# Performance work log

Hardware: AMD Instinct MI355X
Metric: run time of the kernel (lower is better)

Reference implementation:

```python
import jax, jax.numpy as jnp
import numpy as np

NEG = -1e30  # log-space 'zero'


def _lse3(a, b, c):
    m = jnp.maximum(jnp.maximum(a, b), c)
    return m + jnp.log(jnp.exp(a - m) + jnp.exp(b - m) + jnp.exp(c - m))


def _ctc_loss_sum(logp, targets, input_lens, target_lens, blank=0):
    # logp: (T, B, C) log-probabilities; targets: (B, S) int; lens: (B,) int
    T, B, C = logp.shape
    S = targets.shape[1]
    L = 2 * S + 1
    # Extended label sequence: blank, t0, blank, t1, ..., blank  -> (B, L)
    ext = jnp.full((B, L), blank, dtype=targets.dtype).at[:, 1::2].set(targets)
    # Skip transition (l-2 -> l) allowed only for non-blank labels differing from l-2
    allow_skip = jnp.concatenate(
        [jnp.zeros((B, 2), bool), (ext[:, 2:] != blank) & (ext[:, 2:] != ext[:, :-2])],
        axis=1)  # (B, L)
    pos = jnp.arange(L)[None, :]
    valid = pos < (2 * target_lens[:, None] + 1)  # (B, L) mask of used trellis columns

    def emit(lp_t):  # (B, C) -> (B, L): log-prob of emitting ext label at each position
        return jnp.take_along_axis(lp_t, ext, axis=1)

    e0 = emit(logp[0])
    alpha0 = jnp.full((B, L), NEG, logp.dtype).at[:, 0].set(e0[:, 0]).at[:, 1].set(e0[:, 1])
    alpha0 = jnp.where(valid, alpha0, NEG)

    def step(alpha, lp_t):
        a1 = jnp.pad(alpha[:, :-1], ((0, 0), (1, 0)), constant_values=NEG)
        a2 = jnp.pad(alpha[:, :-2], ((0, 0), (2, 0)), constant_values=NEG)
        a2 = jnp.where(allow_skip, a2, NEG)
        new = _lse3(alpha, a1, a2) + emit(lp_t)
        new = jnp.where(valid, new, NEG)
        return new, new

    _, alphas = jax.lax.scan(step, alpha0, logp[1:])
    alphas = jnp.concatenate([alpha0[None], alphas], axis=0)  # (T, B, L)

    # Per-sequence final alpha at t = input_len - 1
    a_fin = alphas[input_lens - 1, jnp.arange(B)]  # (B, L)
    end_blank = jnp.take_along_axis(a_fin, (2 * target_lens)[:, None], axis=1)[:, 0]
    end_label = jnp.take_along_axis(a_fin, (2 * target_lens - 1)[:, None], axis=1)[:, 0]
    m = jnp.maximum(end_blank, end_label)
    loss = -(m + jnp.log(jnp.exp(end_blank - m) + jnp.exp(end_label - m)))  # (B,)
    # zero_infinity=True: replace (near-)infinite losses with 0
    loss = jnp.where(loss > -0.5 * NEG, 0.0, loss)
    # reduction='none' followed by .sum() in the module
    return loss.sum()


def setup_inputs() -> dict:
    key = jax.random.key(0)
    T, B, C, S = 1000, 32, 1000, 100
    k1, k2 = jax.random.split(key)
    logits = jax.random.normal(k1, (T, B, C), dtype=jnp.float32)
    logp = jax.nn.log_softmax(logits, axis=-1)  # CTCLoss expects log-softmax input
    targets = jax.random.randint(k2, (B, S), 1, C)  # labels in [1, C), never blank(0)
    input_lens = jnp.full((B,), T, dtype=jnp.int32)
    target_lens = jnp.full((B,), S, dtype=jnp.int32)
    return {"logp": logp, "targets": targets, "input_lens": input_lens, "target_lens": target_lens}


def reference(logp, targets, input_lens, target_lens):
    return _ctc_loss_sum(logp, targets, input_lens, target_lens, blank=0)
```

## Files before the change

### kernel.cpp

```cpp
#include <hip/hip_runtime.h>
#include <hip/hip_fp16.h>


constexpr int T = 1000, B = 32, C = 1000, S = 100;
constexpr int L = 2 * S + 1;
constexpr int RS = 204;
constexpr int PFD = 32;
constexpr int RROWS = T + PFD;
constexpr float OFF = 7.0f;
constexpr float LOG2E = 1.4426950408889634f;
constexpr float LN2 = 0.6931471805599453f;

__device__ __forceinline__ float dpp_shr1(float x) {
    return __int_as_float(
        __builtin_amdgcn_update_dpp(0, __float_as_int(x), 0x138, 0xF, 0xF, true));
}

__device__ __forceinline__ float wave_max_nonneg(float x) {
#define DPP_MAX(ctrl)                                                        \
    x = fmaxf(x, __int_as_float(__builtin_amdgcn_update_dpp(                 \
                     0, __float_as_int(x), (ctrl), 0xF, 0xF, true)))
    DPP_MAX(0x111);
    DPP_MAX(0x112);
    DPP_MAX(0x114);
    DPP_MAX(0x118);
    DPP_MAX(0x142);
    DPP_MAX(0x143);
#undef DPP_MAX
    return __int_as_float(__builtin_amdgcn_readlane(__float_as_int(x), 63));
}

__global__ void __launch_bounds__(256) stage_kernel(
        const float* __restrict__ logp, const int* __restrict__ targets,
        float* __restrict__ ws) {
    const int t = blockIdx.x * 4 + (threadIdx.x >> 6);
    const int b = blockIdx.y;
    const int lane = threadIdx.x & 63;
    if (lane > 50) return;
    const int col = 4 * lane;
    const float* row = logp + ((size_t)t * B + b) * C;

    const float pb = exp2f((row[0] + OFF) * LOG2E);
    float p1 = 0.f, p3 = 0.f;
    const int l1 = col + 1;
    if (l1 < L) p1 = exp2f((row[targets[b * S + (l1 >> 1)]] + OFF) * LOG2E);
    const int l3 = col + 3;
    if (l3 < L) p3 = exp2f((row[targets[b * S + (l3 >> 1)]] + OFF) * LOG2E);

    float4 v;
    v.x = pb;
    v.y = p1;
    v.z = (col + 2 < L) ? pb : 0.f;
    v.w = p3;
    *reinterpret_cast<float4*>(ws + ((size_t)b * RROWS + t) * RS + col) = v;
}

__global__ void __launch_bounds__(64, 1) ctc_kernel(
        const float* __restrict__ ws, const int* __restrict__ targets,
        const int* __restrict__ input_lens, const int* __restrict__ target_lens,
        float* __restrict__ out) {
    const int b = blockIdx.x;
    const int lane = threadIdx.x;
    const int col = (lane <= 50) ? 4 * lane : 200;
    const int Tb = input_lens[b];
    const int tl = target_lens[b];
    const float* pw = ws + (size_t)b * RROWS * RS;

    float m1 = 0.f, m3 = 0.f;
    if (lane <= 50) {
        const int l1 = col + 1;
        if (l1 >= 3 && l1 < L) {
            const int s = (l1 - 1) >> 1;
            if (targets[b * S + s] != targets[b * S + s - 1]) m1 = 1.f;
        }
        const int l3 = col + 3;
        if (l3 >= 3 && l3 < L) {
            const int s = (l3 - 1) >> 1;
            if (targets[b * S + s] != targets[b * S + s - 1]) m3 = 1.f;
        }
    }

    float a0 = 0.f, a1 = 0.f, a2 = 0.f, a3 = 0.f;
    {
        const float4 q0 = *reinterpret_cast<const float4*>(pw + col);
        if (lane == 0) { a0 = q0.x; a1 = q0.y; }
    }
    int esum = 0;

#define CTC_STEP(Q_)                                  \
    do {                                              \
        const float am1 = dpp_shr1(a3);               \
        const float s01 = a0 + a1;                    \
        const float s23 = a2 + a3;                    \
        const float n0 = (a0 + am1) * (Q_).x;         \
        const float n1 = fmaf(am1, m1, s01) * (Q_).y; \
        const float n2 = (a1 + a2) * (Q_).z;          \
        const float n3 = fmaf(a1, m3, s23) * (Q_).w;  \
        a0 = n0; a1 = n1; a2 = n2; a3 = n3;           \
    } while (0)

#define CTC_RESCALE()                                                          \
    do {                                                                       \
        const float mx = wave_max_nonneg(fmaxf(fmaxf(a0, a1), fmaxf(a2, a3))); \
        const unsigned bits = __float_as_uint(mx);                             \
        if (bits != 0u) {                                                      \
            const int e = (int)((bits >> 23) & 0xFFu) - 127;                   \
            const float sc = __uint_as_float((unsigned)(127 - e) << 23);       \
            a0 *= sc; a1 *= sc; a2 *= sc; a3 *= sc;                            \
            esum += e;                                                         \
        }                                                                      \
    } while (0)

    float4 P[PFD];
    {
        const float* pf0 = pw + (size_t)RS + col;
#pragma unroll
        for (int i = 0; i < PFD; ++i)
            P[i] = *reinterpret_cast<const float4*>(pf0 + (size_t)i * RS);
    }
    const float* pf = pw + (size_t)(PFD + 1) * RS + col;

    int t = 1;
    while (t + PFD <= Tb) {
#pragma unroll
        for (int i = 0; i < PFD; ++i) {
            const float4 q = P[i];
            P[i] = *reinterpret_cast<const float4*>(pf);
            pf += RS;
            CTC_STEP(q);
            if (i == 15) CTC_RESCALE();
        }
        CTC_RESCALE();
        t += PFD;
    }
    {
        const int rem = Tb - t;
#pragma unroll
        for (int i = 0; i < PFD; ++i) {
            if (i < rem) {
                const float4 q = P[i];
                CTC_STEP(q);
                if (i == 15) CTC_RESCALE();
            }
        }
    }
#undef CTC_STEP

    const int e1 = 2 * tl, e2 = 2 * tl - 1;
    float contrib = 0.f;
    if (lane <= 50) {
        if (col + 0 == e1 || col + 0 == e2) contrib += a0;
        if (col + 1 == e1 || col + 1 == e2) contrib += a1;
        if (col + 2 == e1 || col + 2 == e2) contrib += a2;
        if (col + 3 == e1 || col + 3 == e2) contrib += a3;
    }
#pragma unroll
    for (int off = 32; off; off >>= 1) contrib += __shfl_xor(contrib, off);

    if (lane == 0) {
        const float logalpha = logf(contrib) + (float)esum * LN2 - OFF * (float)Tb;
        float loss = -logalpha;
        if (!(loss < 0.5e30f)) loss = 0.f;
        atomicAdd(out, loss);
    }
}

__global__ void __launch_bounds__(64, 1) ctc_direct_kernel(
        const float* __restrict__ logp, const int* __restrict__ targets,
        const int* __restrict__ input_lens, const int* __restrict__ target_lens,
        float* __restrict__ out) {
    const int b = blockIdx.x;
    const int lane = threadIdx.x;
    const int col = (lane <= 50) ? 4 * lane : 200;
    const int Tb = input_lens[b];
    const int tl = target_lens[b];

    int cc[4]; float mm[4], pm[4];
#pragma unroll
    for (int i = 0; i < 4; ++i) {
        const int l = col + i;
        const bool real = (lane <= 50) && (l < L);
        pm[i] = real ? 1.f : 0.f;
        cc[i] = real ? ((l & 1) ? targets[b * S + (l >> 1)] : 0) : 0;
        float mk = 0.f;
        if (real && (l & 1) && l >= 3) {
            const int s = (l - 1) >> 1;
            if (targets[b * S + s] != targets[b * S + s - 1]) mk = 1.f;
        }
        mm[i] = mk;
    }
    const float m1 = mm[1], m3 = mm[3];

    float a0 = 0.f, a1 = 0.f, a2 = 0.f, a3 = 0.f;
    {
        const float* rowp = logp + (size_t)b * C;
        const float p0 = pm[0] * exp2f((rowp[cc[0]] + OFF) * LOG2E);
        const float p1 = pm[1] * exp2f((rowp[cc[1]] + OFF) * LOG2E);
        if (lane == 0) { a0 = p0; a1 = p1; }
    }
    int esum = 0;

    for (int t = 1; t < Tb; ++t) {
        const float* rowp = logp + ((size_t)t * B + b) * C;
        const float p0 = pm[0] * exp2f((rowp[cc[0]] + OFF) * LOG2E);
        const float p1 = pm[1] * exp2f((rowp[cc[1]] + OFF) * LOG2E);
        const float p2 = pm[2] * exp2f((rowp[cc[2]] + OFF) * LOG2E);
        const float p3 = pm[3] * exp2f((rowp[cc[3]] + OFF) * LOG2E);
        const float am1 = dpp_shr1(a3);
        const float n0 = (a0 + am1) * p0;
        const float n1 = fmaf(am1, m1, a0 + a1) * p1;
        const float n2 = (a1 + a2) * p2;
        const float n3 = fmaf(a1, m3, a2 + a3) * p3;
        a0 = n0; a1 = n1; a2 = n2; a3 = n3;
        if ((t & 15) == 0) {
            const float mx = wave_max_nonneg(fmaxf(fmaxf(a0, a1), fmaxf(a2, a3)));
            const unsigned bits = __float_as_uint(mx);
            if (bits != 0u) {
                const int e = (int)((bits >> 23) & 0xFFu) - 127;
                const float sc = __uint_as_float((unsigned)(127 - e) << 23);
                a0 *= sc; a1 *= sc; a2 *= sc; a3 *= sc;
                esum += e;
            }
        }
    }

    const int e1 = 2 * tl, e2 = 2 * tl - 1;
    float contrib = 0.f;
    if (lane <= 50) {
        if (col + 0 == e1 || col + 0 == e2) contrib += a0;
        if (col + 1 == e1 || col + 1 == e2) contrib += a1;
        if (col + 2 == e1 || col + 2 == e2) contrib += a2;
        if (col + 3 == e1 || col + 3 == e2) contrib += a3;
    }
#pragma unroll
    for (int off = 32; off; off >>= 1) contrib += __shfl_xor(contrib, off);
    if (lane == 0) {
        const float logalpha = logf(contrib) + (float)esum * LN2 - OFF * (float)Tb;
        float loss = -logalpha;
        if (!(loss < 0.5e30f)) loss = 0.f;
        atomicAdd(out, loss);
    }
}

extern "C" void kernel_launch(void* const* d_in, const int* in_sizes, int n_in,
                              void* d_out, int out_size, void* d_ws, size_t ws_size,
                              hipStream_t stream) {
    (void)in_sizes; (void)n_in; (void)out_size;
    const float* logp = (const float*)d_in[0];
    const int* targets = (const int*)d_in[1];
    const int* input_lens = (const int*)d_in[2];
    const int* target_lens = (const int*)d_in[3];
    float* out = (float*)d_out;
    float* ws = (float*)d_ws;

    hipMemsetAsync(d_out, 0, sizeof(float), stream);

    const size_t ws_needed = (size_t)B * RROWS * RS * sizeof(float);
    if (ws_size >= ws_needed) {
        dim3 gA(T / 4, B);
        stage_kernel<<<gA, 256, 0, stream>>>(logp, targets, ws);
        ctc_kernel<<<B, 64, 0, stream>>>(ws, targets, input_lens, target_lens, out);
    } else {
        ctc_direct_kernel<<<B, 64, 0, stream>>>(logp, targets, input_lens,
                                                target_lens, out);
    }
}
```

Measured before the change: 234.9 us.

## Merge staging and CTC recursion into one cooperative kernel with grid sync

Replaces the memset plus the two launches (staging kernel, recursion kernel) with a single cooperative kernel. Each of its 1024 waves stages a contiguous time segment for one batch item, then a grid sync hands off to 32 waves that run the recursion, and a second grid sync precedes a deterministic serial sum of the losses. This removes launch gaps and the atomic/memset, but grid syncs have their own cost and staging now uses only 256 blocks. The old multi-kernel path remains as a fallback if the cooperative launch fails.

New measurement: 308.1 us. 1.31x slower.

```diff
diff --git a/kernel.cpp b/kernel.cpp
--- a/kernel.cpp
+++ b/kernel.cpp
@@ -1,6 +1,8 @@
 #include <hip/hip_runtime.h>
-#include <hip/hip_fp16.h>
-
+#include <hip/hip_cooperative_groups.h>
+
+
+namespace cg = cooperative_groups;
 
 constexpr int T = 1000, B = 32, C = 1000, S = 100;
 constexpr int L = 2 * S + 1;
@@ -10,6 +12,15 @@
 constexpr float OFF = 7.0f;
 constexpr float LOG2E = 1.4426950408889634f;
 constexpr float LN2 = 0.6931471805599453f;
+
+constexpr int GBLK = 256;
+constexpr int WPB = 4;
+constexpr int NW = GBLK * WPB;
+constexpr int WAVES_PER_B = NW / B;
+constexpr int TSEG = (T + WAVES_PER_B - 1) / WAVES_PER_B;
+static_assert(NW % B == 0, "wave mapping");
+
+constexpr size_t DATA_WORDS = (size_t)B * RROWS * RS;
 
 __device__ __forceinline__ float dpp_shr1(float x) {
     return __int_as_float(
@@ -30,41 +41,10 @@
     return __int_as_float(__builtin_amdgcn_readlane(__float_as_int(x), 63));
 }
 
-__global__ void __launch_bounds__(256) stage_kernel(
-        const float* __restrict__ logp, const int* __restrict__ targets,
-        float* __restrict__ ws) {
-    const int t = blockIdx.x * 4 + (threadIdx.x >> 6);
-    const int b = blockIdx.y;
-    const int lane = threadIdx.x & 63;
-    if (lane > 50) return;
-    const int col = 4 * lane;
-    const float* row = logp + ((size_t)t * B + b) * C;
-
-    const float pb = exp2f((row[0] + OFF) * LOG2E);
-    float p1 = 0.f, p3 = 0.f;
-    const int l1 = col + 1;
-    if (l1 < L) p1 = exp2f((row[targets[b * S + (l1 >> 1)]] + OFF) * LOG2E);
-    const int l3 = col + 3;
-    if (l3 < L) p3 = exp2f((row[targets[b * S + (l3 >> 1)]] + OFF) * LOG2E);
-
-    float4 v;
-    v.x = pb;
-    v.y = p1;
-    v.z = (col + 2 < L) ? pb : 0.f;
-    v.w = p3;
-    *reinterpret_cast<float4*>(ws + ((size_t)b * RROWS + t) * RS + col) = v;
-}
-
-__global__ void __launch_bounds__(64, 1) ctc_kernel(
-        const float* __restrict__ ws, const int* __restrict__ targets,
-        const int* __restrict__ input_lens, const int* __restrict__ target_lens,
-        float* __restrict__ out) {
-    const int b = blockIdx.x;
-    const int lane = threadIdx.x;
+__device__ float ctc_wave_loss(const float* __restrict__ pw,
+                               const int* __restrict__ targets, int b, int Tb,
+                               int tl, int lane) {
     const int col = (lane <= 50) ? 4 * lane : 200;
-    const int Tb = input_lens[b];
-    const int tl = target_lens[b];
-    const float* pw = ws + (size_t)b * RROWS * RS;
 
     float m1 = 0.f, m3 = 0.f;
     if (lane <= 50) {
@@ -145,6 +125,7 @@
         }
     }
 #undef CTC_STEP
+#undef CTC_RESCALE
 
     const int e1 = 2 * tl, e2 = 2 * tl - 1;
     float contrib = 0.f;
@@ -157,12 +138,119 @@
 #pragma unroll
     for (int off = 32; off; off >>= 1) contrib += __shfl_xor(contrib, off);
 
-    if (lane == 0) {
-        const float logalpha = logf(contrib) + (float)esum * LN2 - OFF * (float)Tb;
-        float loss = -logalpha;
-        if (!(loss < 0.5e30f)) loss = 0.f;
-        atomicAdd(out, loss);
-    }
+    const float logalpha = logf(contrib) + (float)esum * LN2 - OFF * (float)Tb;
+    float loss = -logalpha;
+    if (!(loss < 0.5e30f)) loss = 0.f;
+    return loss;
+}
+
+__global__ void __launch_bounds__(256, 1) ctc_coop_kernel(
+        const float* __restrict__ logp, const int* __restrict__ targets,
+        const int* __restrict__ input_lens, const int* __restrict__ target_lens,
+        float* __restrict__ ws, float* __restrict__ out) {
+    const int lane = threadIdx.x & 63;
+    const int wv = threadIdx.x >> 6;
+    float* loss_slot = ws + DATA_WORDS;
+
+    {
+        const int gw = blockIdx.x * WPB + wv;
+        const int b = gw / WAVES_PER_B;
+        const int seg = gw % WAVES_PER_B;
+        const int t0 = seg * TSEG;
+        const int t1 = min(t0 + TSEG, T);
+        const int col = 4 * lane;
+        const bool ln = (lane <= 50);
+        const bool h1 = ln && (col + 1 < L);
+        const bool h3 = ln && (col + 3 < L);
+        const int c1 = h1 ? targets[b * S + 2 * lane] : 0;
+        const int c3 = h3 ? targets[b * S + 2 * lane + 1] : 0;
+        float* wb = ws + (size_t)b * RROWS * RS;
+
+        for (int t = t0; t < t1; t += 4) {
+            const int n = min(4, t1 - t);
+            float f0[4], fa[4], fb[4];
+#pragma unroll
+            for (int j = 0; j < 4; ++j) {
+                if (j < n) {
+                    const float* row = logp + ((size_t)(t + j) * B + b) * C;
+                    f0[j] = row[0];
+                    fa[j] = h1 ? row[c1] : 0.f;
+                    fb[j] = h3 ? row[c3] : 0.f;
+                }
+            }
+#pragma unroll
+            for (int j = 0; j < 4; ++j) {
+                if (j < n && ln) {
+                    const float pb = exp2f((f0[j] + OFF) * LOG2E);
+                    const float p1 = h1 ? exp2f((fa[j] + OFF) * LOG2E) : 0.f;
+                    const float p3 = h3 ? exp2f((fb[j] + OFF) * LOG2E) : 0.f;
+                    float4 v;
+                    v.x = pb;
+                    v.y = p1;
+                    v.z = (col + 2 < L) ? pb : 0.f;
+                    v.w = p3;
+                    *reinterpret_cast<float4*>(wb + (size_t)(t + j) * RS + col) = v;
+                }
+            }
+        }
+    }
+
+    cg::this_grid().sync();
+
+    if (blockIdx.x < (unsigned)B && wv == 0) {
+        const int b = blockIdx.x;
+        const int Tb = min(input_lens[b], T);
+        const int tl = target_lens[b];
+        const float* pw = ws + (size_t)b * RROWS * RS;
+        const float loss = ctc_wave_loss(pw, targets, b, Tb, tl, lane);
+        if (lane == 0) loss_slot[b] = loss;
+    }
+
+    cg::this_grid().sync();
+
+    if (blockIdx.x == 0 && threadIdx.x == 0) {
+        float s = 0.f;
+        for (int i = 0; i < B; ++i) s += loss_slot[i];
+        out[0] = s;
+    }
+}
+
+__global__ void __launch_bounds__(256) stage_kernel(
+        const float* __restrict__ logp, const int* __restrict__ targets,
+        float* __restrict__ ws) {
+    const int t = blockIdx.x * 4 + (threadIdx.x >> 6);
+    const int b = blockIdx.y;
+    const int lane = threadIdx.x & 63;
+    if (lane > 50) return;
+    const int col = 4 * lane;
+    const float* row = logp + ((size_t)t * B + b) * C;
+
+    const float pb = exp2f((row[0] + OFF) * LOG2E);
+    float p1 = 0.f, p3 = 0.f;
+    const int l1 = col + 1;
+    if (l1 < L) p1 = exp2f((row[targets[b * S + (l1 >> 1)]] + OFF) * LOG2E);
+    const int l3 = col + 3;
+    if (l3 < L) p3 = exp2f((row[targets[b * S + (l3 >> 1)]] + OFF) * LOG2E);
+
+    float4 v;
+    v.x = pb;
+    v.y = p1;
+    v.z = (col + 2 < L) ? pb : 0.f;
+    v.w = p3;
+    *reinterpret_cast<float4*>(ws + ((size_t)b * RROWS + t) * RS + col) = v;
+}
+
+__global__ void __launch_bounds__(64, 1) ctc_kernel(
+        const float* __restrict__ ws, const int* __restrict__ targets,
+        const int* __restrict__ input_lens, const int* __restrict__ target_lens,
+        float* __restrict__ out) {
+    const int b = blockIdx.x;
+    const int lane = threadIdx.x;
+    const int Tb = input_lens[b];
+    const int tl = target_lens[b];
+    const float* pw = ws + (size_t)b * RROWS * RS;
+    const float loss = ctc_wave_loss(pw, targets, b, Tb, tl, lane);
+    if (lane == 0) atomicAdd(out, loss);
 }
 
 __global__ void __launch_bounds__(64, 1) ctc_direct_kernel(
@@ -253,14 +341,19 @@
     float* out = (float*)d_out;
     float* ws = (float*)d_ws;
 
-    hipMemsetAsync(d_out, 0, sizeof(float), stream);
-
-    const size_t ws_needed = (size_t)B * RROWS * RS * sizeof(float);
+    const size_t ws_needed = (DATA_WORDS + (size_t)B) * sizeof(float);
     if (ws_size >= ws_needed) {
+        void* args[] = {(void*)&logp, (void*)&targets, (void*)&input_lens,
+                        (void*)&target_lens, (void*)&ws, (void*)&out};
+        const hipError_t err = hipLaunchCooperativeKernel(
+            (const void*)ctc_coop_kernel, dim3(GBLK), dim3(256), args, 0, stream);
+        if (err == hipSuccess) return;
+        hipMemsetAsync(d_out, 0, sizeof(float), stream);
         dim3 gA(T / 4, B);
         stage_kernel<<<gA, 256, 0, stream>>>(logp, targets, ws);
         ctc_kernel<<<B, 64, 0, stream>>>(ws, targets, input_lens, target_lens, out);
     } else {
+        hipMemsetAsync(d_out, 0, sizeof(float), stream);
         ctc_direct_kernel<<<B, 64, 0, stream>>>(logp, targets, input_lens,
                                                 target_lens, out);
     }
```

## Stage logp rows through LDS with coalesced loads and fold output zeroing

Applied to the files above, without the earlier changes.

The staging kernel now assigns one block per (t,b) row. It copies the full 1000-float row into shared memory with coalesced float4 loads and computes each trellis column's scaled probability from LDS, writing one float per thread. This replaces the previous scattered global gathers of target entries. The output memset is folded into the staging kernel, which saves an API call/launch, and Tb is clamped to T. The trade-off is that the whole row is read (about 4KB versus roughly 400B of gathers), and the grid uses four times as many blocks, each with many idle threads.

Measured after the change: 228.7 us. 2.6% less time.

```diff
diff --git a/kernel.cpp b/kernel.cpp
--- a/kernel.cpp
+++ b/kernel.cpp
@@ -1,5 +1,4 @@
 #include <hip/hip_runtime.h>
-#include <hip/hip_fp16.h>
 
 
 constexpr int T = 1000, B = 32, C = 1000, S = 100;
@@ -10,6 +9,8 @@
 constexpr float OFF = 7.0f;
 constexpr float LOG2E = 1.4426950408889634f;
 constexpr float LN2 = 0.6931471805599453f;
+
+constexpr size_t DATA_WORDS = (size_t)B * RROWS * RS;
 
 __device__ __forceinline__ float dpp_shr1(float x) {
     return __int_as_float(
@@ -32,27 +33,27 @@
 
 __global__ void __launch_bounds__(256) stage_kernel(
         const float* __restrict__ logp, const int* __restrict__ targets,
-        float* __restrict__ ws) {
-    const int t = blockIdx.x * 4 + (threadIdx.x >> 6);
+        float* __restrict__ ws, float* __restrict__ out) {
+    const int t = blockIdx.x;
     const int b = blockIdx.y;
-    const int lane = threadIdx.x & 63;
-    if (lane > 50) return;
-    const int col = 4 * lane;
-    const float* row = logp + ((size_t)t * B + b) * C;
-
-    const float pb = exp2f((row[0] + OFF) * LOG2E);
-    float p1 = 0.f, p3 = 0.f;
-    const int l1 = col + 1;
-    if (l1 < L) p1 = exp2f((row[targets[b * S + (l1 >> 1)]] + OFF) * LOG2E);
-    const int l3 = col + 3;
-    if (l3 < L) p3 = exp2f((row[targets[b * S + (l3 >> 1)]] + OFF) * LOG2E);
-
-    float4 v;
-    v.x = pb;
-    v.y = p1;
-    v.z = (col + 2 < L) ? pb : 0.f;
-    v.w = p3;
-    *reinterpret_cast<float4*>(ws + ((size_t)b * RROWS + t) * RS + col) = v;
+    __shared__ float row[C];
+    const float* src = logp + ((size_t)t * B + b) * C;
+    const int tid = threadIdx.x;
+    if (tid < C / 4) {
+        ((float4*)row)[tid] = ((const float4*)src)[tid];
+    }
+    __syncthreads();
+    if (t == 0 && b == 0 && tid == 0) out[0] = 0.f;
+    if (tid < RS) {
+        float p;
+        if (tid < L) {
+            const int c = (tid & 1) ? targets[b * S + (tid >> 1)] : 0;
+            p = exp2f((row[c] + OFF) * LOG2E);
+        } else {
+            p = 0.0f;
+        }
+        ws[((size_t)b * RROWS + t) * RS + tid] = p;
+    }
 }
 
 __global__ void __launch_bounds__(64, 1) ctc_kernel(
@@ -62,7 +63,7 @@
     const int b = blockIdx.x;
     const int lane = threadIdx.x;
     const int col = (lane <= 50) ? 4 * lane : 200;
-    const int Tb = input_lens[b];
+    const int Tb = min(input_lens[b], T);
     const int tl = target_lens[b];
     const float* pw = ws + (size_t)b * RROWS * RS;
 
@@ -145,6 +146,7 @@
         }
     }
 #undef CTC_STEP
+#undef CTC_RESCALE
 
     const int e1 = 2 * tl, e2 = 2 * tl - 1;
     float contrib = 0.f;
@@ -253,14 +255,13 @@
     float* out = (float*)d_out;
     float* ws = (float*)d_ws;
 
-    hipMemsetAsync(d_out, 0, sizeof(float), stream);
-
-    const size_t ws_needed = (size_t)B * RROWS * RS * sizeof(float);
+    const size_t ws_needed = DATA_WORDS * sizeof(float);
     if (ws_size >= ws_needed) {
-        dim3 gA(T / 4, B);
-        stage_kernel<<<gA, 256, 0, stream>>>(logp, targets, ws);
+        dim3 gA(T, B);
+        stage_kernel<<<gA, 256, 0, stream>>>(logp, targets, ws, out);
         ctc_kernel<<<B, 64, 0, stream>>>(ws, targets, input_lens, target_lens, out);
     } else {
+        hipMemsetAsync(d_out, 0, sizeof(float), stream);
         ctc_direct_kernel<<<B, 64, 0, stream>>>(logp, targets, input_lens,
                                                 target_lens, out);
     }
```
